# Performance work log

Measured on AMD Instinct MI355X. Metric: run time of the kernel, lower is better.

Reference implementation:

```python
import jax, jax.numpy as jnp
import numpy as np

N_NODES = 50000
N_EDGES = 800000
N_GRAPHS = 512
IN_FEATS = 256
HIDDEN = 128
OUT_FEATS = 128


def _lin(key, fan_in, fan_out):
    return jax.random.normal(key, (fan_in, fan_out), jnp.float32) * (1.0 / np.sqrt(fan_in))


def setup_inputs() -> dict:
    key = jax.random.key(0)
    ks = jax.random.split(key, 16)
    x = jax.random.normal(ks[0], (N_NODES, IN_FEATS), jnp.float32)
    edge_index = jax.random.randint(ks[1], (2, N_EDGES), 0, N_NODES, jnp.int32)
    batch = jnp.sort(jax.random.randint(ks[2], (N_NODES,), 0, N_GRAPHS, jnp.int32))
    return {
        "x": x,
        "edge_index": edge_index,
        "batch": batch,
        "num_graphs": N_GRAPHS,
        # TD branch GCN params
        "td_W1": _lin(ks[3], IN_FEATS, HIDDEN), "td_b1": jnp.zeros((HIDDEN,), jnp.float32),
        "td_W2": _lin(ks[4], HIDDEN, OUT_FEATS), "td_b2": jnp.zeros((OUT_FEATS,), jnp.float32),
        # BU branch GCN params
        "bu_W1": _lin(ks[5], IN_FEATS, HIDDEN), "bu_b1": jnp.zeros((HIDDEN,), jnp.float32),
        "bu_W2": _lin(ks[6], HIDDEN, OUT_FEATS), "bu_b2": jnp.zeros((OUT_FEATS,), jnp.float32),
        # proj_head: Linear(256,256) -> ReLU -> Linear(256,128)
        "pw1": _lin(ks[7], OUT_FEATS * 2, 256), "pb1": jnp.zeros((256,), jnp.float32),
        "pw2": _lin(ks[8], 256, 128), "pb2": jnp.zeros((128,), jnp.float32),
    }


def gcn_conv(h_in, W, b, src, dst, n_nodes):
    """PyG GCNConv: self-loops + symmetric normalization D^-1/2 (A+I) D^-1/2 X W + b."""
    h = h_in @ W  # [N, out]
    ones = jnp.ones(src.shape[0], h.dtype)
    deg = jax.ops.segment_sum(ones, dst, num_segments=n_nodes) + 1.0  # +1 for self-loop
    dinv = jax.lax.rsqrt(deg)  # deg >= 1 always
    norm = dinv[src] * dinv[dst]  # [E]
    agg = jax.ops.segment_sum(h[src] * norm[:, None], dst, num_segments=n_nodes)
    agg = agg + h * (dinv * dinv)[:, None]  # self-loop edge contribution
    return agg + b


def reference(x, edge_index, batch, num_graphs,
              td_W1, td_b1, td_W2, td_b2,
              bu_W1, bu_b1, bu_W2, bu_b2,
              pw1, pb1, pw2, pb2):
    n = x.shape[0]
    src, dst = edge_index[0], edge_index[1]

    def branch(W1, b1, W2, b2, s, d):
        h = jax.nn.relu(gcn_conv(x, W1, b1, s, d, n))
        # dropout is identity in eval mode
        h = gcn_conv(h, W2, b2, s, d, n)
        return jax.ops.segment_sum(h, batch, num_segments=num_graphs)  # global_add_pool

    td = branch(td_W1, td_b1, td_W2, td_b2, src, dst)
    bu = branch(bu_W1, bu_b1, bu_W2, bu_b2, dst, src)  # flipped edge_index
    h = jnp.concatenate([bu, td], axis=1)  # [G, 2*out_feats]
    h = jax.nn.relu(h @ pw1 + pb1) @ pw2 + pb2
    return h
```

## Files before the change

kernel.cpp:

```cpp
#include <hip/hip_runtime.h>

#define N_NODES 50000
#define N_PAD   50048
#define N_EDGES 800000
#define N_GRAPHS 512
#define F_IN 256
#define F_H 128
#define F_CAT 256

#define BSHIFT 9
#define NB 98
#define CAP 10240
#define EPB 3125

typedef __attribute__((ext_vector_type(8))) short short8;
typedef __attribute__((ext_vector_type(4))) float f32x4;
typedef unsigned int uint;
typedef unsigned short ushort;

static __device__ __forceinline__ ushort f2bf(float f) {
    uint u = __float_as_uint(f);
    u += 0x7FFF + ((u >> 16) & 1);
    return (ushort)(u >> 16);
}
static __device__ __forceinline__ float bflo(uint v) { return __uint_as_float(v << 16); }
static __device__ __forceinline__ float bfhi(uint v) { return __uint_as_float(v & 0xFFFF0000u); }

#define GLL(g, l) __builtin_amdgcn_global_load_lds( \
    (const __attribute__((address_space(1))) unsigned int*)(g), \
    (__attribute__((address_space(3))) unsigned int*)(l), 16, 0, 0)

__global__ __launch_bounds__(256) void csr_scatter_kernel(
        const int* __restrict__ ei, int* __restrict__ gcur,
        uint* __restrict__ ebuf_td, uint* __restrict__ ebuf_bu) {
    __shared__ int lcnt[256];
    __shared__ int lbase[256];
    int tid = threadIdx.x;
    lcnt[tid] = 0;
    __syncthreads();
    int e0 = blockIdx.x * EPB;
    for (int k = tid; k < EPB; k += 256) {
        int i = e0 + k;
        int s = ei[i], d = ei[N_EDGES + i];
        atomicAdd(&lcnt[d >> BSHIFT], 1);
        atomicAdd(&lcnt[128 + (s >> BSHIFT)], 1);
    }
    __syncthreads();
    if (tid < 2 * NB) {
        int dir = tid / NB, b = tid % NB;
        int c = lcnt[dir * 128 + b];
        lbase[dir * 128 + b] = c ? atomicAdd(&gcur[dir * NB + b], c) : 0;
    }
    __syncthreads();
    lcnt[tid] = 0;
    __syncthreads();
    for (int k = tid; k < EPB; k += 256) {
        int i = e0 + k;
        int s = ei[i], d = ei[N_EDGES + i];
        int bd = d >> BSHIFT, bs = s >> BSHIFT;
        int p = atomicAdd(&lcnt[bd], 1) + lbase[bd];
        ebuf_td[(size_t)bd * CAP + p] = (uint)s | ((uint)(d & 511) << 16);
        int q = atomicAdd(&lcnt[128 + bs], 1) + lbase[128 + bs];
        ebuf_bu[(size_t)bs * CAP + q] = (uint)d | ((uint)(s & 511) << 16);
    }
}

__global__ __launch_bounds__(256) void csr_build_kernel(
        const uint* __restrict__ ebuf_td, const uint* __restrict__ ebuf_bu,
        const int* __restrict__ gcur,
        int* off_td, int* off_bu, ushort* deg_td, ushort* deg_bu,
        float* dinv_td, float* dinv_bu, ushort* csr_td, ushort* csr_bu) {
    int b = blockIdx.x, dir = blockIdx.y;
    const uint* ebuf = dir ? ebuf_bu : ebuf_td;
    int* off     = dir ? off_bu : off_td;
    ushort* deg  = dir ? deg_bu : deg_td;
    float* dinv  = dir ? dinv_bu : dinv_td;
    ushort* csr  = dir ? csr_bu : csr_td;
    __shared__ int cntL[512], offL[512], sm[256];
    int tid = threadIdx.x;
    cntL[tid] = 0; cntL[tid + 256] = 0;
    __syncthreads();
    int rbeg = b * CAP;
    int rend = rbeg + gcur[dir * NB + b];
    for (int k = rbeg + tid; k < rend; k += 256)
        atomicAdd(&cntL[ebuf[k] >> 16], 1);
    __syncthreads();
    int a0 = cntL[tid * 2], a1 = cntL[tid * 2 + 1];
    int ps = a0 + a1;
    sm[tid] = ps;
    __syncthreads();
    for (int o = 1; o < 256; o <<= 1) {
        int u = (tid >= o) ? sm[tid - o] : 0;
        __syncthreads();
        sm[tid] += u;
        __syncthreads();
    }
    int excl = sm[tid] - ps;
    offL[tid * 2] = excl;
    offL[tid * 2 + 1] = excl + a0;
    __syncthreads();
    int nbase = b << BSHIFT;
#pragma unroll
    for (int j = 0; j < 2; j++) {
        int nloc = tid + j * 256;
        int n = nbase + nloc;
        if (n < N_NODES) {
            off[n] = rbeg + offL[nloc];
            int c = cntL[nloc];
            deg[n] = (ushort)c;
            dinv[n] = rsqrtf((float)c + 1.0f);
        }
    }
    cntL[tid] = offL[tid];
    cntL[tid + 256] = offL[tid + 256];
    __syncthreads();
    for (int k = rbeg + tid; k < rend; k += 256) {
        uint e = ebuf[k];
        int slot = atomicAdd(&cntL[e >> 16], 1);
        csr[rbeg + slot] = (ushort)(e & 0xFFFF);
    }
}

__global__ void cvt_x_kernel(const float* __restrict__ x, ushort* __restrict__ xb) {
    size_t i = (size_t)blockIdx.x * blockDim.x + threadIdx.x;
    ushort4 u = {0, 0, 0, 0};
    if (i < (size_t)N_NODES * (F_IN / 4)) {
        float4 f = ((const float4*)x)[i];
        u.x = f2bf(f.x); u.y = f2bf(f.y); u.z = f2bf(f.z); u.w = f2bf(f.w);
    }
    ((ushort4*)xb)[i] = u;
}

__global__ void prep_w_kernel(const float* __restrict__ td_W1, const float* __restrict__ bu_W1,
                              const float* __restrict__ td_W2, const float* __restrict__ bu_W2,
                              ushort* __restrict__ Bt1, ushort* __restrict__ Bt2) {
    int n = blockIdx.x;
    int k = threadIdx.x;
    float w1 = (n < F_H) ? td_W1[(size_t)k * F_H + n] : bu_W1[(size_t)k * F_H + (n - F_H)];
    Bt1[(size_t)n * 256 + k] = f2bf(w1);
    if (k < 128) {
        float w2 = (n < F_H) ? td_W2[(size_t)k * F_H + n]
                             : bu_W2[(size_t)k * F_H + (n - F_H)];
        Bt2[(size_t)n * 128 + k] = f2bf(w2);
    }
}

__global__ __launch_bounds__(256) void gemm_mfma(
        const ushort* __restrict__ A, const ushort* __restrict__ Bt,
        ushort* __restrict__ C,
        const float* __restrict__ dinv_td, const float* __restrict__ dinv_bu,
        int kLen, int ldb, int aSplit) {
    __shared__ __align__(16) ushort As[128 * 32];
    __shared__ __align__(16) ushort Bs[128 * 32];
    int tid = threadIdx.x;
    int wave = tid >> 6, lane = tid & 63, quad = lane >> 4, l16 = lane & 15;
    size_t bm = (size_t)blockIdx.x * 128;
    size_t bn = (size_t)blockIdx.y * 128;
    const float* dsel = blockIdx.y ? dinv_bu : dinv_td;
    int aOff = aSplit ? (int)bn : 0;

    f32x4 acc[2][8];
    const f32x4 z4 = {0.f, 0.f, 0.f, 0.f};
#pragma unroll
    for (int i = 0; i < 2; i++)
#pragma unroll
        for (int j = 0; j < 8; j++) acc[i][j] = z4;

    int cb0 = wave * 64;
    int cb1 = 256 + wave * 64;
    int c0 = cb0 + lane, c1 = cb1 + lane;
    int r0 = c0 >> 2, s0 = (c0 & 3) * 8;
    int r1 = c1 >> 2, s1 = (c1 & 3) * 8;
    const ushort* a0p = A + (bm + r0) * 256 + aOff + s0;
    const ushort* a1p = A + (bm + r1) * 256 + aOff + s1;
    const ushort* b0p = Bt + (bn + r0) * ldb + s0;
    const ushort* b1p = Bt + (bn + r1) * ldb + s1;
    ushort* lA0 = As + cb0 * 8;
    ushort* lA1 = As + cb1 * 8;
    ushort* lB0 = Bs + cb0 * 8;
    ushort* lB1 = Bs + cb1 * 8;

    int nkb = kLen >> 5;
    for (int kb = 0; kb < nkb; kb++) {
        int k0 = kb * 32;
        __syncthreads();
        GLL(a0p + k0, lA0);
        GLL(a1p + k0, lA1);
        GLL(b0p + k0, lB0);
        GLL(b1p + k0, lB1);
        __syncthreads();
        short8 af0 = *(const short8*)(As + (wave * 32 + l16) * 32 + quad * 8);
        short8 af1 = *(const short8*)(As + (wave * 32 + 16 + l16) * 32 + quad * 8);
#pragma unroll
        for (int ct = 0; ct < 8; ct++) {
            short8 bfr = *(const short8*)(Bs + (ct * 16 + l16) * 32 + quad * 8);
            acc[0][ct] = __builtin_amdgcn_mfma_f32_16x16x32_bf16(af0, bfr, acc[0][ct], 0, 0, 0);
            acc[1][ct] = __builtin_amdgcn_mfma_f32_16x16x32_bf16(af1, bfr, acc[1][ct], 0, 0, 0);
        }
    }
#pragma unroll
    for (int rt = 0; rt < 2; rt++) {
#pragma unroll
        for (int r = 0; r < 4; r++) {
            size_t row = bm + wave * 32 + rt * 16 + quad * 4 + r;
            float dv = dsel[row];
#pragma unroll
            for (int ct = 0; ct < 8; ct++) {
                C[row * 256 + bn + ct * 16 + l16] = f2bf(acc[rt][ct][r] * dv);
            }
        }
    }
}

static __device__ __forceinline__ void gather_node(
        const ushort* __restrict__ base, const ushort* __restrict__ csr,
        int kb, int ke, int half, float a[4]) {
    float p[4] = {0.f, 0.f, 0.f, 0.f};
    float q[4] = {0.f, 0.f, 0.f, 0.f};
    float r[4] = {0.f, 0.f, 0.f, 0.f};
    int k = kb;
    for (; k + 8 <= ke; k += 8) {
        int i0 = csr[k + half];
        int i1 = csr[k + 2 + half];
        int i2 = csr[k + 4 + half];
        int i3 = csr[k + 6 + half];
        uint2 v0 = *(const uint2*)(base + (size_t)i0 * F_CAT);
        uint2 v1 = *(const uint2*)(base + (size_t)i1 * F_CAT);
        uint2 v2 = *(const uint2*)(base + (size_t)i2 * F_CAT);
        uint2 v3 = *(const uint2*)(base + (size_t)i3 * F_CAT);
        a[0] += bflo(v0.x); a[1] += bfhi(v0.x); a[2] += bflo(v0.y); a[3] += bfhi(v0.y);
        p[0] += bflo(v1.x); p[1] += bfhi(v1.x); p[2] += bflo(v1.y); p[3] += bfhi(v1.y);
        q[0] += bflo(v2.x); q[1] += bfhi(v2.x); q[2] += bflo(v2.y); q[3] += bfhi(v2.y);
        r[0] += bflo(v3.x); r[1] += bfhi(v3.x); r[2] += bflo(v3.y); r[3] += bfhi(v3.y);
    }
    for (; k < ke; k += 2) {
        int kk = k + half;
        if (kk < ke) {
            uint2 v = *(const uint2*)(base + (size_t)csr[kk] * F_CAT);
            a[0] += bflo(v.x); a[1] += bfhi(v.x); a[2] += bflo(v.y); a[3] += bfhi(v.y);
        }
    }
#pragma unroll
    for (int j = 0; j < 4; j++) a[j] += (p[j] + q[j]) + r[j];
}

__global__ __launch_bounds__(256) void agg1_kernel(
        const ushort* __restrict__ linS, ushort* __restrict__ h1b,
        const ushort* __restrict__ csr_td, const int* __restrict__ off_td,
        const ushort* __restrict__ deg_td, const float* __restrict__ dinv_td,
        const ushort* __restrict__ csr_bu, const int* __restrict__ off_bu,
        const ushort* __restrict__ deg_bu, const float* __restrict__ dinv_bu,
        const float* __restrict__ b_td, const float* __restrict__ b_bu) {
    int wave = threadIdx.x >> 6, lane = threadIdx.x & 63;
    int n = blockIdx.x * 2 + (wave >> 1);
    int br = wave & 1;
    const ushort* csr = br ? csr_bu : csr_td;
    const int* off    = br ? off_bu : off_td;
    const ushort* deg = br ? deg_bu : deg_td;
    const float* dinv = br ? dinv_bu : dinv_td;
    const float* bias = br ? b_bu : b_td;
    int half = lane >> 5, l32 = lane & 31;
    int col = br * F_H + l32 * 4;
    const ushort* base = linS + col;

    float a[4] = {0.f, 0.f, 0.f, 0.f};
    int kb = off[n];
    gather_node(base, csr, kb, kb + deg[n], half, a);
#pragma unroll
    for (int j = 0; j < 4; j++) a[j] += __shfl_xor(a[j], 32);
    uint2 vs = *(const uint2*)(base + (size_t)n * F_CAT);
    a[0] += bflo(vs.x); a[1] += bfhi(vs.x); a[2] += bflo(vs.y); a[3] += bfhi(vs.y);
    float dn = dinv[n];
    int bcol = l32 * 4;
    float o0 = fmaxf(a[0] * dn + bias[bcol],     0.f);
    float o1 = fmaxf(a[1] * dn + bias[bcol + 1], 0.f);
    float o2 = fmaxf(a[2] * dn + bias[bcol + 2], 0.f);
    float o3 = fmaxf(a[3] * dn + bias[bcol + 3], 0.f);
    if (half == 0) {
        uint2 pk;
        pk.x = (uint)f2bf(o0) | ((uint)f2bf(o1) << 16);
        pk.y = (uint)f2bf(o2) | ((uint)f2bf(o3) << 16);
        *(uint2*)(h1b + (size_t)n * F_CAT + col) = pk;
    }
}

__global__ __launch_bounds__(256) void agg2_pool_kernel(
        const ushort* __restrict__ linS, float* __restrict__ pooled,
        const int* __restrict__ batch,
        const ushort* __restrict__ csr_td, const int* __restrict__ off_td,
        const ushort* __restrict__ deg_td, const float* __restrict__ dinv_td,
        const ushort* __restrict__ csr_bu, const int* __restrict__ off_bu,
        const ushort* __restrict__ deg_bu, const float* __restrict__ dinv_bu,
        const float* __restrict__ b_td, const float* __restrict__ b_bu) {
    int wave = threadIdx.x >> 6, lane = threadIdx.x & 63;
    int n0 = (blockIdx.x * 2 + (wave >> 1)) * 8;
    int br = wave & 1;
    const ushort* csr = br ? csr_bu : csr_td;
    const int* off    = br ? off_bu : off_td;
    const ushort* deg = br ? deg_bu : deg_td;
    const float* dinv = br ? dinv_bu : dinv_td;
    const float* bias = br ? b_bu : b_td;
    int half = lane >> 5, l32 = lane & 31;
    int col = br * F_H + l32 * 4;
    int pcol = (br ? 0 : F_H) + l32 * 4;
    const ushort* base = linS + col;
    int bcol = l32 * 4;
    float bs0 = bias[bcol], bs1 = bias[bcol + 1];
    float bs2 = bias[bcol + 2], bs3 = bias[bcol + 3];

    float acc0 = 0.f, acc1 = 0.f, acc2 = 0.f, acc3 = 0.f;
    int gcur = batch[n0];
#pragma unroll
    for (int j = 0; j < 8; j++) {
        int n = n0 + j;
        int g = batch[n];
        if (g != gcur) {
            if (half == 0) {
                float* pp = &pooled[(size_t)gcur * F_CAT + pcol];
                unsafeAtomicAdd(pp,     acc0);
                unsafeAtomicAdd(pp + 1, acc1);
                unsafeAtomicAdd(pp + 2, acc2);
                unsafeAtomicAdd(pp + 3, acc3);
            }
            acc0 = acc1 = acc2 = acc3 = 0.f;
            gcur = g;
        }
        float a[4] = {0.f, 0.f, 0.f, 0.f};
        int kb = off[n];
        gather_node(base, csr, kb, kb + deg[n], half, a);
#pragma unroll
        for (int t = 0; t < 4; t++) a[t] += __shfl_xor(a[t], 32);
        uint2 vs = *(const uint2*)(base + (size_t)n * F_CAT);
        a[0] += bflo(vs.x); a[1] += bfhi(vs.x); a[2] += bflo(vs.y); a[3] += bfhi(vs.y);
        float dn = dinv[n];
        acc0 += a[0] * dn + bs0;
        acc1 += a[1] * dn + bs1;
        acc2 += a[2] * dn + bs2;
        acc3 += a[3] * dn + bs3;
    }
    if (half == 0) {
        float* pp = &pooled[(size_t)gcur * F_CAT + pcol];
        unsafeAtomicAdd(pp,     acc0);
        unsafeAtomicAdd(pp + 1, acc1);
        unsafeAtomicAdd(pp + 2, acc2);
        unsafeAtomicAdd(pp + 3, acc3);
    }
}

__global__ __launch_bounds__(256) void mlp_kernel(const float* __restrict__ pooled,
                                                  const float* __restrict__ pw1,
                                                  const float* __restrict__ pb1,
                                                  const float* __restrict__ pw2,
                                                  const float* __restrict__ pb2,
                                                  float* __restrict__ out) {
    int g = blockIdx.x;
    int tid = threadIdx.x;
    __shared__ float row[256];
    __shared__ float hid[256];
    row[tid] = pooled[(size_t)g * 256 + tid];
    __syncthreads();
    float acc = pb1[tid];
    for (int k = 0; k < 256; k++) acc += row[k] * pw1[(size_t)k * 256 + tid];
    hid[tid] = fmaxf(acc, 0.f);
    __syncthreads();
    if (tid < 128) {
        float o = pb2[tid];
        for (int k = 0; k < 256; k++) o += hid[k] * pw2[(size_t)k * 128 + tid];
        out[(size_t)g * 128 + tid] = o;
    }
}

extern "C" void kernel_launch(void* const* d_in, const int* in_sizes, int n_in,
                              void* d_out, int out_size, void* d_ws, size_t ws_size,
                              hipStream_t stream) {
    const float* x     = (const float*)d_in[0];
    const int*   ei    = (const int*)d_in[1];
    const int*   batch = (const int*)d_in[2];
    const float* td_W1 = (const float*)d_in[4];
    const float* td_b1 = (const float*)d_in[5];
    const float* td_W2 = (const float*)d_in[6];
    const float* td_b2 = (const float*)d_in[7];
    const float* bu_W1 = (const float*)d_in[8];
    const float* bu_b1 = (const float*)d_in[9];
    const float* bu_W2 = (const float*)d_in[10];
    const float* bu_b2 = (const float*)d_in[11];
    const float* pw1   = (const float*)d_in[12];
    const float* pb1   = (const float*)d_in[13];
    const float* pw2   = (const float*)d_in[14];
    const float* pb2   = (const float*)d_in[15];
    float* out = (float*)d_out;

    char* p = (char*)d_ws;
    auto alloc = [&](size_t bytes) { void* r = (void*)p; p += (bytes + 255) & ~(size_t)255; return r; };
    char* zreg = (char*)alloc(1024 + (size_t)N_GRAPHS * F_CAT * sizeof(float));
    int* gcur = (int*)zreg;
    float* pooled = (float*)(zreg + 1024);
    uint* ebuf_td = (uint*)alloc((size_t)NB * CAP * sizeof(uint));
    uint* ebuf_bu = (uint*)alloc((size_t)NB * CAP * sizeof(uint));
    ushort* csr_td = (ushort*)alloc((size_t)NB * CAP * sizeof(ushort));
    ushort* csr_bu = (ushort*)alloc((size_t)NB * CAP * sizeof(ushort));
    int* off_td = (int*)alloc((size_t)N_NODES * sizeof(int));
    int* off_bu = (int*)alloc((size_t)N_NODES * sizeof(int));
    ushort* deg_td = (ushort*)alloc((size_t)N_NODES * sizeof(ushort));
    ushort* deg_bu = (ushort*)alloc((size_t)N_NODES * sizeof(ushort));
    float* dinv_td = (float*)alloc((size_t)N_PAD * sizeof(float));
    float* dinv_bu = (float*)alloc((size_t)N_PAD * sizeof(float));
    ushort* Bt1 = (ushort*)alloc((size_t)256 * 256 * sizeof(ushort));
    ushort* Bt2 = (ushort*)alloc((size_t)256 * 128 * sizeof(ushort));
    ushort* xb   = (ushort*)alloc((size_t)N_PAD * F_CAT * sizeof(ushort));
    ushort* linb = (ushort*)alloc((size_t)N_PAD * F_CAT * sizeof(ushort));
    ushort* h1b  = (ushort*)alloc((size_t)N_PAD * F_CAT * sizeof(ushort));

    hipMemsetAsync(zreg, 0, 1024 + (size_t)N_GRAPHS * F_CAT * sizeof(float), stream);

    csr_scatter_kernel<<<N_EDGES / EPB, 256, 0, stream>>>(ei, gcur, ebuf_td, ebuf_bu);
    csr_build_kernel<<<dim3(NB, 2), 256, 0, stream>>>(ebuf_td, ebuf_bu, gcur,
        off_td, off_bu, deg_td, deg_bu, dinv_td, dinv_bu, csr_td, csr_bu);

    cvt_x_kernel<<<(N_PAD * F_IN / 4) / 256, 256, 0, stream>>>(x, xb);
    prep_w_kernel<<<256, 256, 0, stream>>>(td_W1, bu_W1, td_W2, bu_W2, Bt1, Bt2);

    dim3 gg(N_PAD / 128, 2);

    gemm_mfma<<<gg, 256, 0, stream>>>(xb, Bt1, linb, dinv_td, dinv_bu, 256, 256, 0);
    agg1_kernel<<<N_NODES / 2, 256, 0, stream>>>(linb, h1b,
        csr_td, off_td, deg_td, dinv_td, csr_bu, off_bu, deg_bu, dinv_bu, td_b1, bu_b1);

    gemm_mfma<<<gg, 256, 0, stream>>>(h1b, Bt2, linb, dinv_td, dinv_bu, 128, 128, 1);
    agg2_pool_kernel<<<N_NODES / 16, 256, 0, stream>>>(linb, pooled, batch,
        csr_td, off_td, deg_td, dinv_td, csr_bu, off_bu, deg_bu, dinv_bu, td_b2, bu_b2);

    mlp_kernel<<<N_GRAPHS, 256, 0, stream>>>(pooled, pw1, pb1, pw2, pb2, out);
}
```

Baseline: 360.9 us.

## Move layer-2 weight multiply after pooling to drop second node-level GEMM

Because aggregation and pooling are linear, the second GCN layer's W2 multiply is applied after global pooling on 512 graph rows instead of on all 50k nodes. This removes the second MFMA GEMM launch and its full-size intermediate write/read. Layer-1 output is prescaled by dinv so layer-2 aggregation runs on 128-wide h1 directly, with the bias scaled by node count, which comes from a binary search over batch. It also widens the gather unroll to 16 and processes 8 nodes per wave in agg1. Bias and rounding order change slightly, with bf16 W2 applied to fp32 pooled sums.

```diff
diff --git a/kernel.cpp b/kernel.cpp
--- a/kernel.cpp
+++ b/kernel.cpp
@@ -25,6 +25,7 @@
 }
 static __device__ __forceinline__ float bflo(uint v) { return __uint_as_float(v << 16); }
 static __device__ __forceinline__ float bfhi(uint v) { return __uint_as_float(v & 0xFFFF0000u); }
+static __device__ __forceinline__ float bfu(ushort v) { return __uint_as_float((uint)v << 16); }
 
 #define GLL(g, l) __builtin_amdgcn_global_load_lds( \
     (const __attribute__((address_space(1))) unsigned int*)(g), \
@@ -133,23 +134,22 @@
 
 __global__ void prep_w_kernel(const float* __restrict__ td_W1, const float* __restrict__ bu_W1,
                               const float* __restrict__ td_W2, const float* __restrict__ bu_W2,
-                              ushort* __restrict__ Bt1, ushort* __restrict__ Bt2) {
+                              ushort* __restrict__ Bt1, ushort* __restrict__ Wt2) {
     int n = blockIdx.x;
     int k = threadIdx.x;
     float w1 = (n < F_H) ? td_W1[(size_t)k * F_H + n] : bu_W1[(size_t)k * F_H + (n - F_H)];
     Bt1[(size_t)n * 256 + k] = f2bf(w1);
     if (k < 128) {
-        float w2 = (n < F_H) ? td_W2[(size_t)k * F_H + n]
-                             : bu_W2[(size_t)k * F_H + (n - F_H)];
-        Bt2[(size_t)n * 128 + k] = f2bf(w2);
+        float w2 = (n < F_H) ? bu_W2[(size_t)k * F_H + n]
+                             : td_W2[(size_t)k * F_H + (n - F_H)];
+        Wt2[(size_t)k * 256 + n] = f2bf(w2);
     }
 }
 
 __global__ __launch_bounds__(256) void gemm_mfma(
         const ushort* __restrict__ A, const ushort* __restrict__ Bt,
         ushort* __restrict__ C,
-        const float* __restrict__ dinv_td, const float* __restrict__ dinv_bu,
-        int kLen, int ldb, int aSplit) {
+        const float* __restrict__ dinv_td, const float* __restrict__ dinv_bu) {
     __shared__ __align__(16) ushort As[128 * 32];
     __shared__ __align__(16) ushort Bs[128 * 32];
     int tid = threadIdx.x;
@@ -157,7 +157,6 @@
     size_t bm = (size_t)blockIdx.x * 128;
     size_t bn = (size_t)blockIdx.y * 128;
     const float* dsel = blockIdx.y ? dinv_bu : dinv_td;
-    int aOff = aSplit ? (int)bn : 0;
 
     f32x4 acc[2][8];
     const f32x4 z4 = {0.f, 0.f, 0.f, 0.f};
@@ -171,17 +170,16 @@
     int c0 = cb0 + lane, c1 = cb1 + lane;
     int r0 = c0 >> 2, s0 = (c0 & 3) * 8;
     int r1 = c1 >> 2, s1 = (c1 & 3) * 8;
-    const ushort* a0p = A + (bm + r0) * 256 + aOff + s0;
-    const ushort* a1p = A + (bm + r1) * 256 + aOff + s1;
-    const ushort* b0p = Bt + (bn + r0) * ldb + s0;
-    const ushort* b1p = Bt + (bn + r1) * ldb + s1;
+    const ushort* a0p = A + (bm + r0) * 256 + s0;
+    const ushort* a1p = A + (bm + r1) * 256 + s1;
+    const ushort* b0p = Bt + (bn + r0) * 256 + s0;
+    const ushort* b1p = Bt + (bn + r1) * 256 + s1;
     ushort* lA0 = As + cb0 * 8;
     ushort* lA1 = As + cb1 * 8;
     ushort* lB0 = Bs + cb0 * 8;
     ushort* lB1 = Bs + cb1 * 8;
 
-    int nkb = kLen >> 5;
-    for (int kb = 0; kb < nkb; kb++) {
+    for (int kb = 0; kb < 8; kb++) {
         int k0 = kb * 32;
         __syncthreads();
         GLL(a0p + k0, lA0);
@@ -219,11 +217,31 @@
     float q[4] = {0.f, 0.f, 0.f, 0.f};
     float r[4] = {0.f, 0.f, 0.f, 0.f};
     int k = kb;
+    for (; k + 16 <= ke; k += 16) {
+        int i0 = csr[k + half],      i1 = csr[k + 2 + half];
+        int i2 = csr[k + 4 + half],  i3 = csr[k + 6 + half];
+        int i4 = csr[k + 8 + half],  i5 = csr[k + 10 + half];
+        int i6 = csr[k + 12 + half], i7 = csr[k + 14 + half];
+        uint2 v0 = *(const uint2*)(base + (size_t)i0 * F_CAT);
+        uint2 v1 = *(const uint2*)(base + (size_t)i1 * F_CAT);
+        uint2 v2 = *(const uint2*)(base + (size_t)i2 * F_CAT);
+        uint2 v3 = *(const uint2*)(base + (size_t)i3 * F_CAT);
+        uint2 v4 = *(const uint2*)(base + (size_t)i4 * F_CAT);
+        uint2 v5 = *(const uint2*)(base + (size_t)i5 * F_CAT);
+        uint2 v6 = *(const uint2*)(base + (size_t)i6 * F_CAT);
+        uint2 v7 = *(const uint2*)(base + (size_t)i7 * F_CAT);
+        a[0] += bflo(v0.x); a[1] += bfhi(v0.x); a[2] += bflo(v0.y); a[3] += bfhi(v0.y);
+        p[0] += bflo(v1.x); p[1] += bfhi(v1.x); p[2] += bflo(v1.y); p[3] += bfhi(v1.y);
+        q[0] += bflo(v2.x); q[1] += bfhi(v2.x); q[2] += bflo(v2.y); q[3] += bfhi(v2.y);
+        r[0] += bflo(v3.x); r[1] += bfhi(v3.x); r[2] += bflo(v3.y); r[3] += bfhi(v3.y);
+        a[0] += bflo(v4.x); a[1] += bfhi(v4.x); a[2] += bflo(v4.y); a[3] += bfhi(v4.y);
+        p[0] += bflo(v5.x); p[1] += bfhi(v5.x); p[2] += bflo(v5.y); p[3] += bfhi(v5.y);
+        q[0] += bflo(v6.x); q[1] += bfhi(v6.x); q[2] += bflo(v6.y); q[3] += bfhi(v6.y);
+        r[0] += bflo(v7.x); r[1] += bfhi(v7.x); r[2] += bflo(v7.y); r[3] += bfhi(v7.y);
+    }
     for (; k + 8 <= ke; k += 8) {
-        int i0 = csr[k + half];
-        int i1 = csr[k + 2 + half];
-        int i2 = csr[k + 4 + half];
-        int i3 = csr[k + 6 + half];
+        int i0 = csr[k + half],     i1 = csr[k + 2 + half];
+        int i2 = csr[k + 4 + half], i3 = csr[k + 6 + half];
         uint2 v0 = *(const uint2*)(base + (size_t)i0 * F_CAT);
         uint2 v1 = *(const uint2*)(base + (size_t)i1 * F_CAT);
         uint2 v2 = *(const uint2*)(base + (size_t)i2 * F_CAT);
@@ -245,48 +263,7 @@
 }
 
 __global__ __launch_bounds__(256) void agg1_kernel(
-        const ushort* __restrict__ linS, ushort* __restrict__ h1b,
-        const ushort* __restrict__ csr_td, const int* __restrict__ off_td,
-        const ushort* __restrict__ deg_td, const float* __restrict__ dinv_td,
-        const ushort* __restrict__ csr_bu, const int* __restrict__ off_bu,
-        const ushort* __restrict__ deg_bu, const float* __restrict__ dinv_bu,
-        const float* __restrict__ b_td, const float* __restrict__ b_bu) {
-    int wave = threadIdx.x >> 6, lane = threadIdx.x & 63;
-    int n = blockIdx.x * 2 + (wave >> 1);
-    int br = wave & 1;
-    const ushort* csr = br ? csr_bu : csr_td;
-    const int* off    = br ? off_bu : off_td;
-    const ushort* deg = br ? deg_bu : deg_td;
-    const float* dinv = br ? dinv_bu : dinv_td;
-    const float* bias = br ? b_bu : b_td;
-    int half = lane >> 5, l32 = lane & 31;
-    int col = br * F_H + l32 * 4;
-    const ushort* base = linS + col;
-
-    float a[4] = {0.f, 0.f, 0.f, 0.f};
-    int kb = off[n];
-    gather_node(base, csr, kb, kb + deg[n], half, a);
-#pragma unroll
-    for (int j = 0; j < 4; j++) a[j] += __shfl_xor(a[j], 32);
-    uint2 vs = *(const uint2*)(base + (size_t)n * F_CAT);
-    a[0] += bflo(vs.x); a[1] += bfhi(vs.x); a[2] += bflo(vs.y); a[3] += bfhi(vs.y);
-    float dn = dinv[n];
-    int bcol = l32 * 4;
-    float o0 = fmaxf(a[0] * dn + bias[bcol],     0.f);
-    float o1 = fmaxf(a[1] * dn + bias[bcol + 1], 0.f);
-    float o2 = fmaxf(a[2] * dn + bias[bcol + 2], 0.f);
-    float o3 = fmaxf(a[3] * dn + bias[bcol + 3], 0.f);
-    if (half == 0) {
-        uint2 pk;
-        pk.x = (uint)f2bf(o0) | ((uint)f2bf(o1) << 16);
-        pk.y = (uint)f2bf(o2) | ((uint)f2bf(o3) << 16);
-        *(uint2*)(h1b + (size_t)n * F_CAT + col) = pk;
-    }
-}
-
-__global__ __launch_bounds__(256) void agg2_pool_kernel(
-        const ushort* __restrict__ linS, float* __restrict__ pooled,
-        const int* __restrict__ batch,
+        const ushort* __restrict__ linS, ushort* __restrict__ h1s,
         const ushort* __restrict__ csr_td, const int* __restrict__ off_td,
         const ushort* __restrict__ deg_td, const float* __restrict__ dinv_td,
         const ushort* __restrict__ csr_bu, const int* __restrict__ off_bu,
@@ -302,11 +279,52 @@
     const float* bias = br ? b_bu : b_td;
     int half = lane >> 5, l32 = lane & 31;
     int col = br * F_H + l32 * 4;
-    int pcol = (br ? 0 : F_H) + l32 * 4;
     const ushort* base = linS + col;
     int bcol = l32 * 4;
     float bs0 = bias[bcol], bs1 = bias[bcol + 1];
     float bs2 = bias[bcol + 2], bs3 = bias[bcol + 3];
+
+#pragma unroll
+    for (int j = 0; j < 8; j++) {
+        int n = n0 + j;
+        float a[4] = {0.f, 0.f, 0.f, 0.f};
+        int kb = off[n];
+        gather_node(base, csr, kb, kb + deg[n], half, a);
+#pragma unroll
+        for (int t = 0; t < 4; t++) a[t] += __shfl_xor(a[t], 32);
+        uint2 vs = *(const uint2*)(base + (size_t)n * F_CAT);
+        a[0] += bflo(vs.x); a[1] += bfhi(vs.x); a[2] += bflo(vs.y); a[3] += bfhi(vs.y);
+        float dn = dinv[n];
+        float o0 = fmaxf(a[0] * dn + bs0, 0.f) * dn;
+        float o1 = fmaxf(a[1] * dn + bs1, 0.f) * dn;
+        float o2 = fmaxf(a[2] * dn + bs2, 0.f) * dn;
+        float o3 = fmaxf(a[3] * dn + bs3, 0.f) * dn;
+        if (half == 0) {
+            uint2 pk;
+            pk.x = (uint)f2bf(o0) | ((uint)f2bf(o1) << 16);
+            pk.y = (uint)f2bf(o2) | ((uint)f2bf(o3) << 16);
+            *(uint2*)(h1s + (size_t)n * F_CAT + col) = pk;
+        }
+    }
+}
+
+__global__ __launch_bounds__(256) void agg2_pool_kernel(
+        const ushort* __restrict__ h1s, float* __restrict__ pooled_pre,
+        const int* __restrict__ batch,
+        const ushort* __restrict__ csr_td, const int* __restrict__ off_td,
+        const ushort* __restrict__ deg_td, const float* __restrict__ dinv_td,
+        const ushort* __restrict__ csr_bu, const int* __restrict__ off_bu,
+        const ushort* __restrict__ deg_bu, const float* __restrict__ dinv_bu) {
+    int wave = threadIdx.x >> 6, lane = threadIdx.x & 63;
+    int n0 = (blockIdx.x * 2 + (wave >> 1)) * 8;
+    int br = wave & 1;
+    const ushort* csr = br ? csr_bu : csr_td;
+    const int* off    = br ? off_bu : off_td;
+    const ushort* deg = br ? deg_bu : deg_td;
+    const float* dinv = br ? dinv_bu : dinv_td;
+    int half = lane >> 5, l32 = lane & 31;
+    int col = br * F_H + l32 * 4;
+    const ushort* base = h1s + col;
 
     float acc0 = 0.f, acc1 = 0.f, acc2 = 0.f, acc3 = 0.f;
     int gcur = batch[n0];
@@ -316,7 +334,7 @@
         int g = batch[n];
         if (g != gcur) {
             if (half == 0) {
-                float* pp = &pooled[(size_t)gcur * F_CAT + pcol];
+                float* pp = &pooled_pre[(size_t)gcur * F_CAT + col];
                 unsafeAtomicAdd(pp,     acc0);
                 unsafeAtomicAdd(pp + 1, acc1);
                 unsafeAtomicAdd(pp + 2, acc2);
@@ -333,13 +351,13 @@
         uint2 vs = *(const uint2*)(base + (size_t)n * F_CAT);
         a[0] += bflo(vs.x); a[1] += bfhi(vs.x); a[2] += bflo(vs.y); a[3] += bfhi(vs.y);
         float dn = dinv[n];
-        acc0 += a[0] * dn + bs0;
-        acc1 += a[1] * dn + bs1;
-        acc2 += a[2] * dn + bs2;
-        acc3 += a[3] * dn + bs3;
+        acc0 += a[0] * dn;
+        acc1 += a[1] * dn;
+        acc2 += a[2] * dn;
+        acc3 += a[3] * dn;
     }
     if (half == 0) {
-        float* pp = &pooled[(size_t)gcur * F_CAT + pcol];
+        float* pp = &pooled_pre[(size_t)gcur * F_CAT + col];
         unsafeAtomicAdd(pp,     acc0);
         unsafeAtomicAdd(pp + 1, acc1);
         unsafeAtomicAdd(pp + 2, acc2);
@@ -347,21 +365,33 @@
     }
 }
 
-__global__ __launch_bounds__(256) void mlp_kernel(const float* __restrict__ pooled,
-                                                  const float* __restrict__ pw1,
-                                                  const float* __restrict__ pb1,
-                                                  const float* __restrict__ pw2,
-                                                  const float* __restrict__ pb2,
-                                                  float* __restrict__ out) {
+__global__ __launch_bounds__(256) void head_kernel(
+        const float* __restrict__ pooled_pre, const int* __restrict__ batch,
+        const ushort* __restrict__ Wt2,
+        const float* __restrict__ td_b2, const float* __restrict__ bu_b2,
+        const float* __restrict__ pw1, const float* __restrict__ pb1,
+        const float* __restrict__ pw2, const float* __restrict__ pb2,
+        float* __restrict__ out) {
     int g = blockIdx.x;
     int tid = threadIdx.x;
-    __shared__ float row[256];
-    __shared__ float hid[256];
-    row[tid] = pooled[(size_t)g * 256 + tid];
-    __syncthreads();
-    float acc = pb1[tid];
-    for (int k = 0; k < 256; k++) acc += row[k] * pw1[(size_t)k * 256 + tid];
-    hid[tid] = fmaxf(acc, 0.f);
+    __shared__ float row[256], z[256], hid[256];
+    row[tid] = pooled_pre[(size_t)g * 256 + tid];
+    int lo = 0, hi = N_NODES;
+    while (lo < hi) { int m = (lo + hi) >> 1; if (batch[m] < g) lo = m + 1; else hi = m; }
+    int start = lo;
+    lo = start; hi = N_NODES;
+    while (lo < hi) { int m = (lo + hi) >> 1; if (batch[m] < g + 1) lo = m + 1; else hi = m; }
+    float cnt = (float)(lo - start);
+    __syncthreads();
+    const float* rsel = (tid < 128) ? (row + F_H) : row;
+    float b2 = (tid < 128) ? bu_b2[tid] : td_b2[tid - F_H];
+    float acc = cnt * b2;
+    for (int k = 0; k < F_H; k++) acc += rsel[k] * bfu(Wt2[(size_t)k * 256 + tid]);
+    z[tid] = acc;
+    __syncthreads();
+    float h = pb1[tid];
+    for (int k = 0; k < 256; k++) h += z[k] * pw1[(size_t)k * 256 + tid];
+    hid[tid] = fmaxf(h, 0.f);
     __syncthreads();
     if (tid < 128) {
         float o = pb2[tid];
@@ -394,7 +424,7 @@
     auto alloc = [&](size_t bytes) { void* r = (void*)p; p += (bytes + 255) & ~(size_t)255; return r; };
     char* zreg = (char*)alloc(1024 + (size_t)N_GRAPHS * F_CAT * sizeof(float));
     int* gcur = (int*)zreg;
-    float* pooled = (float*)(zreg + 1024);
+    float* pooled_pre = (float*)(zreg + 1024);
     uint* ebuf_td = (uint*)alloc((size_t)NB * CAP * sizeof(uint));
     uint* ebuf_bu = (uint*)alloc((size_t)NB * CAP * sizeof(uint));
     ushort* csr_td = (ushort*)alloc((size_t)NB * CAP * sizeof(ushort));
@@ -406,10 +436,10 @@
     float* dinv_td = (float*)alloc((size_t)N_PAD * sizeof(float));
     float* dinv_bu = (float*)alloc((size_t)N_PAD * sizeof(float));
     ushort* Bt1 = (ushort*)alloc((size_t)256 * 256 * sizeof(ushort));
-    ushort* Bt2 = (ushort*)alloc((size_t)256 * 128 * sizeof(ushort));
+    ushort* Wt2 = (ushort*)alloc((size_t)128 * 256 * sizeof(ushort));
     ushort* xb   = (ushort*)alloc((size_t)N_PAD * F_CAT * sizeof(ushort));
     ushort* linb = (ushort*)alloc((size_t)N_PAD * F_CAT * sizeof(ushort));
-    ushort* h1b  = (ushort*)alloc((size_t)N_PAD * F_CAT * sizeof(ushort));
+    ushort* h1s  = (ushort*)alloc((size_t)N_PAD * F_CAT * sizeof(ushort));
 
     hipMemsetAsync(zreg, 0, 1024 + (size_t)N_GRAPHS * F_CAT * sizeof(float), stream);
 
@@ -418,17 +448,16 @@
         off_td, off_bu, deg_td, deg_bu, dinv_td, dinv_bu, csr_td, csr_bu);
 
     cvt_x_kernel<<<(N_PAD * F_IN / 4) / 256, 256, 0, stream>>>(x, xb);
-    prep_w_kernel<<<256, 256, 0, stream>>>(td_W1, bu_W1, td_W2, bu_W2, Bt1, Bt2);
+    prep_w_kernel<<<256, 256, 0, stream>>>(td_W1, bu_W1, td_W2, bu_W2, Bt1, Wt2);
 
     dim3 gg(N_PAD / 128, 2);
-
-    gemm_mfma<<<gg, 256, 0, stream>>>(xb, Bt1, linb, dinv_td, dinv_bu, 256, 256, 0);
-    agg1_kernel<<<N_NODES / 2, 256, 0, stream>>>(linb, h1b,
+    gemm_mfma<<<gg, 256, 0, stream>>>(xb, Bt1, linb, dinv_td, dinv_bu);
+    agg1_kernel<<<N_NODES / 16, 256, 0, stream>>>(linb, h1s,
         csr_td, off_td, deg_td, dinv_td, csr_bu, off_bu, deg_bu, dinv_bu, td_b1, bu_b1);
 
-    gemm_mfma<<<gg, 256, 0, stream>>>(h1b, Bt2, linb, dinv_td, dinv_bu, 128, 128, 1);
-    agg2_pool_kernel<<<N_NODES / 16, 256, 0, stream>>>(linb, pooled, batch,
-        csr_td, off_td, deg_td, dinv_td, csr_bu, off_bu, deg_bu, dinv_bu, td_b2, bu_b2);
-
-    mlp_kernel<<<N_GRAPHS, 256, 0, stream>>>(pooled, pw1, pb1, pw2, pb2, out);
-}
+    agg2_pool_kernel<<<N_NODES / 16, 256, 0, stream>>>(h1s, pooled_pre, batch,
+        csr_td, off_td, deg_td, dinv_td, csr_bu, off_bu, deg_bu, dinv_bu);
+
+    head_kernel<<<N_GRAPHS, 256, 0, stream>>>(pooled_pre, batch, Wt2,
+        td_b2, bu_b2, pw1, pb1, pw2, pb2, out);
+}
```

Result: faster. 351.7 us (-2.6%).
